# Performance work log

Measured on AMD Instinct MI355X. Metric: run time of the kernel, lower is better.

Reference implementation:

```python
import jax, jax.numpy as jnp
import numpy as np

KS = 3            # kernel_size
DILS = (1, 2, 4)  # dilation_list == padding_list
EPS = 1e-5        # BN eps


def _unfold3(x, d):
    # emulate F.unfold(kernel=3, dilation=d, padding=d, stride=1).view(b, c, 9, h, w)
    b, c, h, w = x.shape
    xp = jnp.pad(x, ((0, 0), (0, 0), (d, d), (d, d)))
    pats = [xp[:, :, i * d:i * d + h, j * d:j * d + w] for i in range(KS) for j in range(KS)]
    return jnp.stack(pats, axis=2)


def _conv1x1(x, w, b):
    return jnp.einsum('bchw,oc->bohw', x, w) + b[None, :, None, None]


def _bn_relu(x, g, be, m, v):
    s = g / jnp.sqrt(v + EPS)
    return jax.nn.relu(x * s[None, :, None, None] + (be - m * s)[None, :, None, None])


def _proj(x, w1, b1, g1, be1, m1, v1, w2, b2, g2, be2, m2, v2):
    h = _bn_relu(_conv1x1(x, w1, b1), g1, be1, m1, v1)
    return _bn_relu(_conv1x1(h, w2, b2), g2, be2, m2, v2)


def setup_inputs():
    key = jax.random.key(0)
    Cin, Ck, Cv, Cout = 512, 256, 256, 512
    B, H, W = 4, 64, 64
    ks = iter(jax.random.split(key, 48))

    def nrm(shape, s=0.02):
        return jax.random.normal(next(ks), shape, jnp.float32) * s

    def bn(c):
        return (jnp.ones((c,), jnp.float32) + nrm((c,), 0.1),  # gamma
                nrm((c,), 0.1),                                 # beta
                nrm((c,), 0.1),                                 # running mean
                jax.random.uniform(next(ks), (c,), jnp.float32, 0.5, 1.5))  # running var

    inp = {"x": jax.random.normal(next(ks), (B, Cin, H, W), jnp.float32)}
    for p in ("k", "q"):
        g1, be1, m1, v1 = bn(Ck)
        g2, be2, m2, v2 = bn(Ck)
        inp.update({
            p + "1_w": nrm((Ck, Cin)), p + "1_b": nrm((Ck,)),
            p + "1_g": g1, p + "1_be": be1, p + "1_m": m1, p + "1_v": v1,
            p + "2_w": nrm((Ck, Ck)), p + "2_b": nrm((Ck,)),
            p + "2_g": g2, p + "2_be": be2, p + "2_m": m2, p + "2_v": v2,
        })
    inp["v_w"] = nrm((Cv, Cin)); inp["v_b"] = nrm((Cv,))
    inp["w_w"] = nrm((Cout, Cv)); inp["w_b"] = nrm((Cout,))
    return inp


def reference(x,
              k1_w, k1_b, k1_g, k1_be, k1_m, k1_v,
              k2_w, k2_b, k2_g, k2_be, k2_m, k2_v,
              q1_w, q1_b, q1_g, q1_be, q1_m, q1_v,
              q2_w, q2_b, q2_g, q2_be, q2_m, q2_v,
              v_w, v_b, w_w, w_b):
    # scale == 1: MaxPool2d(1x1-equivalent) and final bilinear resize are identities.
    value = _conv1x1(x, v_w, v_b)                                  # (b,cv,h,w)
    keyf = _proj(x, k1_w, k1_b, k1_g, k1_be, k1_m, k1_v,
                 k2_w, k2_b, k2_g, k2_be, k2_m, k2_v)              # (b,ck,h,w)
    query = _proj(x, q1_w, q1_b, q1_g, q1_be, q1_m, q1_v,
                  q2_w, q2_b, q2_g, q2_be, q2_m, q2_v)             # (b,ck,h,w)
    uk = jnp.concatenate([_unfold3(keyf, d) for d in DILS], axis=2)   # (b,ck,27,h,w)
    uv = jnp.concatenate([_unfold3(value, d) for d in DILS], axis=2)  # (b,cv,27,h,w)
    sim = jnp.sum(uk * query[:, :, None], axis=1, keepdims=True)      # (b,1,27,h,w)
    sim = jax.nn.softmax(sim, axis=2)
    context = jnp.sum(sim * uv, axis=2)                               # (b,cv,h,w)
    return _conv1x1(context, w_w, w_b)
```

## Files before the change

### kernel.cpp

```cpp
#include <hip/hip_runtime.h>

#define HW   4096
#define Hh   64
#define Ww   64
#define NB   27
#define EPSBN 1e-5f

typedef _Float16 f16x8 __attribute__((ext_vector_type(8)));
typedef _Float16 f16x4 __attribute__((ext_vector_type(4)));
typedef _Float16 f16x2 __attribute__((ext_vector_type(2)));
typedef float    f32x4 __attribute__((ext_vector_type(4)));

__device__ __forceinline__ void gld_lds16(const void* g, void* l) {
    __builtin_amdgcn_global_load_lds(
        (const __attribute__((address_space(1))) unsigned int*)g,
        (__attribute__((address_space(3))) unsigned int*)l, 16, 0, 0);
}

struct GJob {
    const _Float16* in;
    const float*    xf;
    const float*    w;
    const float* b; const float* g; const float* be; const float* m; const float* v;
    _Float16* oh;
    float*    of;
};

__global__ __launch_bounds__(512, 1)
void gemm_f(GJob J0, GJob J1, GJob J2, int stage, int K, int JO, int mode)
{
    __shared__ _Float16 As[2][3][4096];
    __shared__ _Float16 Bs[3][16384];

    const int tid  = threadIdx.x;
    const int lane = tid & 63;
    const int w8   = tid >> 6;
    const int lr   = lane & 15;
    const int lg   = lane >> 4;
    const int wq   = w8 & 3;
    const int ph   = w8 >> 2;

    const int bid = blockIdx.x;
    const int xcd = bid & 7;
    const int jj  = bid >> 3;
    const int nb  = xcd * 8 + (jj >> 2);
    const int u   = jj & 3;

    const int nA = (stage == 1) ? 3 : 2;
    int js0, js1, js2, ob0, ob1, ob2;
    if (stage == 1)      { js0 = 0; js1 = 1; js2 = 2; ob0 = ob1 = ob2 = u * 64; }
    else if (stage == 2) { js0 = js1 = js2 = (u >> 1); ob0 = (u & 1) * 128; ob1 = ob0 + 64; ob2 = ob1; }
    else                 { js0 = js1 = js2 = 0; ob0 = u * 128; ob1 = ob0 + 64; ob2 = ob1; }

#define JSEL(js, f) ((js) == 0 ? J0.f : ((js) == 1 ? J1.f : J2.f))
    const float* w0 = JSEL(js0, w);
    const float* w1 = JSEL(js1, w);
    const float* w2 = JSEL(js2, w);
    const float* b0 = JSEL(js0, b); const float* g0 = JSEL(js0, g);
    const float* be0 = JSEL(js0, be); const float* m0 = JSEL(js0, m); const float* v0 = JSEL(js0, v);
    const float* b1 = JSEL(js1, b); const float* g1 = JSEL(js1, g);
    const float* be1 = JSEL(js1, be); const float* m1 = JSEL(js1, m); const float* v1 = JSEL(js1, v);
    const float* b2 = JSEL(js2, b); const float* g2 = JSEL(js2, g);
    const float* be2 = JSEL(js2, be); const float* m2 = JSEL(js2, m); const float* v2 = JSEL(js2, v);
    _Float16* oh0 = JSEL(js0, oh); float* of0 = JSEL(js0, of);
    _Float16* oh1 = JSEL(js1, oh); float* of1 = JSEL(js1, of);
    _Float16* oh2 = JSEL(js2, oh); float* of2 = JSEL(js2, of);
    const _Float16* bIn = JSEL(js0, in);
    const float*    bXf = JSEL(js0, xf);
#undef JSEL

    const int scol = (((lane & 7) ^ (lane >> 3)) << 3);
    const int rowA = w8 * 8 + (lane >> 3);
    const float* aS0 = w0 + (size_t)(ob0 + rowA) * K + scol;
    const float* aS1 = w1 + (size_t)(ob1 + rowA) * K + scol;
    const float* aS2 = w2 + (size_t)(ob2 + rowA) * K + scol;
    const int aoffW  = w8 * 1024 + lane * 16;

    const int rowB = w8 * 32 + (lane >> 3);
    const _Float16* bS = bIn ? (bIn + (size_t)(nb * 256 + rowB) * K + scol) : nullptr;

    const int px   = tid & 255;
    const int chh  = tid >> 8;
    const int pgS  = nb * 256 + px;
    const float* xbase = bXf ? (bXf + (size_t)(pgS >> 12) * 512 * HW + (pgS & 4095)) : nullptr;
    const int bxk  = (px & 7) << 4;
    const bool f32B = (bXf != nullptr);

    float ar0[8], ar1[8], ar2[8];
    float fr[32];

    auto ISSUE_A = [&](int rd) {
        const int kb = rd * 64;
        *(float4*)&ar0[0] = *(const float4*)(aS0 + kb);
        *(float4*)&ar0[4] = *(const float4*)(aS0 + kb + 4);
        *(float4*)&ar1[0] = *(const float4*)(aS1 + kb);
        *(float4*)&ar1[4] = *(const float4*)(aS1 + kb + 4);
        if (nA > 2) {
            *(float4*)&ar2[0] = *(const float4*)(aS2 + kb);
            *(float4*)&ar2[4] = *(const float4*)(aS2 + kb + 4);
        }
    };
    auto WRITE_A = [&](int buf) {
        f16x8 h0, h1, h2;
        #pragma unroll
        for (int i2 = 0; i2 < 8; ++i2) h0[i2] = (_Float16)ar0[i2];
        #pragma unroll
        for (int i2 = 0; i2 < 8; ++i2) h1[i2] = (_Float16)ar1[i2];
        *(f16x8*)((char*)&As[buf][0][0] + aoffW) = h0;
        *(f16x8*)((char*)&As[buf][1][0] + aoffW) = h1;
        if (nA > 2) {
            #pragma unroll
            for (int i2 = 0; i2 < 8; ++i2) h2[i2] = (_Float16)ar2[i2];
            *(f16x8*)((char*)&As[buf][2][0] + aoffW) = h2;
        }
    };
    auto ISSUE_BX = [&](int rd) {
        const int cb = rd * 64 + chh * 32;
        #pragma unroll
        for (int i2 = 0; i2 < 32; ++i2)
            fr[i2] = xbase[(size_t)(cb + i2) * HW];
    };
    auto WRITE_BX = [&](int buf) {
        #pragma unroll
        for (int g4 = 0; g4 < 4; ++g4) {
            f16x8 hv;
            #pragma unroll
            for (int i2 = 0; i2 < 8; ++i2) hv[i2] = (_Float16)fr[g4 * 8 + i2];
            *(f16x8*)((char*)&Bs[buf][0] + px * 128 + ((chh * 64 + g4 * 16) ^ bxk)) = hv;
        }
    };
    auto STAGE_B16 = [&](int buf, int rd) {
        const int kb = rd * 64;
        #pragma unroll
        for (int j2 = 0; j2 < 4; ++j2)
            gld_lds16(bS + (size_t)j2 * 8 * K + kb, (char*)&Bs[buf][0] + w8 * 4096 + j2 * 1024);
    };

    f32x4 acc0[8] = {}, acc1[8] = {}, acc2[8] = {};
    const int nr = K >> 6;

    auto MFMA_TILE = [&](int bb, int ab) {
        #pragma unroll
        for (int ks = 0; ks < 2; ++ks) {
            const int colx = (ks * 64 + lg * 16) ^ ((lr & 7) << 4);
            f16x8 bfr[8];
            #pragma unroll
            for (int t = 0; t < 8; ++t)
                bfr[t] = *(const f16x8*)((const char*)&Bs[bb][0] + (ph * 128 + t * 16 + lr) * 128 + colx);
            const int aoff = (wq * 16 + lr) * 128 + colx;
            const f16x8 af0 = *(const f16x8*)((const char*)&As[ab][0][0] + aoff);
            const f16x8 af1 = *(const f16x8*)((const char*)&As[ab][1][0] + aoff);
            #pragma unroll
            for (int t = 0; t < 8; ++t)
                acc0[t] = __builtin_amdgcn_mfma_f32_16x16x32_f16(af0, bfr[t], acc0[t], 0, 0, 0);
            #pragma unroll
            for (int t = 0; t < 8; ++t)
                acc1[t] = __builtin_amdgcn_mfma_f32_16x16x32_f16(af1, bfr[t], acc1[t], 0, 0, 0);
            if (nA > 2) {
                const f16x8 af2 = *(const f16x8*)((const char*)&As[ab][2][0] + aoff);
                #pragma unroll
                for (int t = 0; t < 8; ++t)
                    acc2[t] = __builtin_amdgcn_mfma_f32_16x16x32_f16(af2, bfr[t], acc2[t], 0, 0, 0);
            }
        }
    };

    if (f32B) {
        ISSUE_A(0);
        ISSUE_BX(0);
        WRITE_BX(0);
        WRITE_A(0);
        __syncthreads();
        int cur = 0;
        for (int rd = 0; rd < nr; ++rd) {
            const bool more = (rd + 1 < nr);
            if (more) {
                ISSUE_A(rd + 1);
                ISSUE_BX(rd + 1);
            }
            MFMA_TILE(cur, cur);
            if (more) {
                WRITE_A(cur ^ 1);
                WRITE_BX(cur ^ 1);
            }
            __syncthreads();
            cur ^= 1;
        }
    } else {
        STAGE_B16(0, 0);
        ISSUE_A(0);
        STAGE_B16(1, 1);
        WRITE_A(0);
        asm volatile("s_waitcnt vmcnt(4) lgkmcnt(0)" ::: "memory");
        __builtin_amdgcn_s_barrier();
        __builtin_amdgcn_sched_barrier(0);

        for (int rd = 0; rd < nr; ++rd) {
            const bool m1 = (rd + 1 < nr);
            const bool m2 = (rd + 2 < nr);
            if (m1) ISSUE_A(rd + 1);
            if (m2) STAGE_B16((rd + 2) % 3, rd + 2);
            MFMA_TILE(rd % 3, rd & 1);
            if (m1) WRITE_A((rd + 1) & 1);
            if (m2) asm volatile("s_waitcnt vmcnt(4) lgkmcnt(0)" ::: "memory");
            else    asm volatile("s_waitcnt vmcnt(0) lgkmcnt(0)" ::: "memory");
            __builtin_amdgcn_s_barrier();
            __builtin_amdgcn_sched_barrier(0);
        }
    }

#define EPI(accS, obS, bS_, gS, beS, mS, vS, ohS, ofS) do {                      \
        const int o4 = (obS) + wq * 16 + lg * 4;                                 \
        float sc[4], off[4];                                                     \
        _Pragma("unroll")                                                        \
        for (int r = 0; r < 4; ++r) {                                            \
            const int o = o4 + r;                                                \
            if (gS) { float s = (gS)[o] * rsqrtf((vS)[o] + EPSBN);               \
                      sc[r] = s; off[r] = fmaf((bS_)[o] - (mS)[o], s, (beS)[o]); }\
            else    { sc[r] = 1.f; off[r] = (bS_)[o]; }                          \
        }                                                                        \
        _Pragma("unroll")                                                        \
        for (int t = 0; t < 8; ++t) {                                            \
            const int pg = nb * 256 + ph * 128 + t * 16 + lr;                    \
            float vv[4];                                                         \
            _Pragma("unroll")                                                    \
            for (int r = 0; r < 4; ++r) {                                        \
                float tv = fmaf(accS[t][r], sc[r], off[r]);                      \
                vv[r] = (gS) ? fmaxf(tv, 0.f) : tv;                              \
            }                                                                    \
            if (mode == 0) {                                                     \
                f16x4 hh;                                                        \
                _Pragma("unroll")                                                \
                for (int r = 0; r < 4; ++r) hh[r] = (_Float16)vv[r];             \
                *(f16x4*)((ohS) + (size_t)pg * JO + o4) = hh;                    \
            } else {                                                             \
                _Pragma("unroll")                                                \
                for (int r = 0; r < 4; ++r)                                      \
                    (ofS)[((size_t)(pg >> 12) * JO + o4 + r) * HW + (pg & 4095)] = vv[r]; \
            }                                                                    \
        }                                                                        \
    } while (0)

    EPI(acc0, ob0, b0, g0, be0, m0, v0, oh0, of0);
    EPI(acc1, ob1, b1, g1, be1, m1, v1, oh1, of1);
    if (nA > 2) EPI(acc2, ob2, b2, g2, be2, m2, v2, oh2, of2);
#undef EPI
}

__global__ __launch_bounds__(256)
void attn_fused(const _Float16* __restrict__ keyT, const _Float16* __restrict__ qryT,
                const _Float16* __restrict__ valT, _Float16* __restrict__ ctxT)
{
    const int tid  = threadIdx.x;
    const int slot = tid & 31;
    const int b    = blockIdx.y;
    const int p    = blockIdx.x * 8 + (tid >> 5);
    const int y    = p >> 6;
    const int xc   = p & 63;

    int   idx[NB];
    float valf[NB];
    #pragma unroll
    for (int n = 0; n < NB; ++n) {
        const int d  = (n < 9) ? 1 : (n < 18 ? 2 : 4);
        const int i  = (n / 3) % 3 - 1;
        const int j  = n % 3 - 1;
        const int yy = y + i * d, xx = xc + j * d;
        const bool ok = ((unsigned)yy < (unsigned)Hh) && ((unsigned)xx < (unsigned)Ww);
        idx[n]  = min(max(yy, 0), Hh - 1) * Ww + min(max(xx, 0), Ww - 1);
        valf[n] = ok ? 1.f : 0.f;
    }

    const size_t base = (size_t)b * HW * 256 + slot * 8;
    const f16x8 q8 = *(const f16x8*)(qryT + base + (size_t)p * 256);

    f16x2 qp[4];
    qp[0] = __builtin_shufflevector(q8, q8, 0, 1);
    qp[1] = __builtin_shufflevector(q8, q8, 2, 3);
    qp[2] = __builtin_shufflevector(q8, q8, 4, 5);
    qp[3] = __builtin_shufflevector(q8, q8, 6, 7);

    float sim[NB];
    #pragma unroll
    for (int n = 0; n < NB; ++n) {
        const f16x8 k8 = *(const f16x8*)(keyT + base + (size_t)idx[n] * 256);
        float s = 0.f;
        s = __builtin_amdgcn_fdot2(__builtin_shufflevector(k8, k8, 0, 1), qp[0], s, false);
        s = __builtin_amdgcn_fdot2(__builtin_shufflevector(k8, k8, 2, 3), qp[1], s, false);
        s = __builtin_amdgcn_fdot2(__builtin_shufflevector(k8, k8, 4, 5), qp[2], s, false);
        s = __builtin_amdgcn_fdot2(__builtin_shufflevector(k8, k8, 6, 7), qp[3], s, false);
        sim[n] = s;
    }

    #pragma unroll
    for (int n = 0; n < NB; ++n) {
        float s = sim[n];
        s += __shfl_xor(s, 1);
        s += __shfl_xor(s, 2);
        s += __shfl_xor(s, 4);
        s += __shfl_xor(s, 8);
        s += __shfl_xor(s, 16);
        sim[n] = s * valf[n];
    }

    float mx = sim[0];
    #pragma unroll
    for (int n = 1; n < NB; ++n) mx = fmaxf(mx, sim[n]);
    float sum = 0.f;
    #pragma unroll
    for (int n = 0; n < NB; ++n) { sim[n] = __expf(sim[n] - mx); sum += sim[n]; }
    const float inv = 1.f / sum;
    #pragma unroll
    for (int n = 0; n < NB; ++n) sim[n] = sim[n] * inv * valf[n];

    float acc[8];
    #pragma unroll
    for (int i = 0; i < 8; ++i) acc[i] = 0.f;
    #pragma unroll
    for (int n = 0; n < NB; ++n) {
        const f16x8 v8 = *(const f16x8*)(valT + base + (size_t)idx[n] * 256);
        const float w = sim[n];
        #pragma unroll
        for (int i = 0; i < 8; ++i) acc[i] = fmaf(w, (float)v8[i], acc[i]);
    }

    f16x8 h;
    #pragma unroll
    for (int i = 0; i < 8; ++i) h[i] = (_Float16)acc[i];
    *(f16x8*)(ctxT + base + (size_t)p * 256) = h;
}

extern "C" void kernel_launch(void* const* d_in, const int* in_sizes, int n_in,
                              void* d_out, int out_size, void* d_ws, size_t ws_size,
                              hipStream_t stream)
{
    (void)in_sizes; (void)n_in; (void)out_size; (void)ws_size;
    const float* x     = (const float*)d_in[0];
    const float* k1_w  = (const float*)d_in[1];
    const float* k1_b  = (const float*)d_in[2];
    const float* k1_g  = (const float*)d_in[3];
    const float* k1_be = (const float*)d_in[4];
    const float* k1_m  = (const float*)d_in[5];
    const float* k1_v  = (const float*)d_in[6];
    const float* k2_w  = (const float*)d_in[7];
    const float* k2_b  = (const float*)d_in[8];
    const float* k2_g  = (const float*)d_in[9];
    const float* k2_be = (const float*)d_in[10];
    const float* k2_m  = (const float*)d_in[11];
    const float* k2_v  = (const float*)d_in[12];
    const float* q1_w  = (const float*)d_in[13];
    const float* q1_b  = (const float*)d_in[14];
    const float* q1_g  = (const float*)d_in[15];
    const float* q1_be = (const float*)d_in[16];
    const float* q1_m  = (const float*)d_in[17];
    const float* q1_v  = (const float*)d_in[18];
    const float* q2_w  = (const float*)d_in[19];
    const float* q2_b  = (const float*)d_in[20];
    const float* q2_g  = (const float*)d_in[21];
    const float* q2_be = (const float*)d_in[22];
    const float* q2_m  = (const float*)d_in[23];
    const float* q2_v  = (const float*)d_in[24];
    const float* v_w   = (const float*)d_in[25];
    const float* v_b   = (const float*)d_in[26];
    const float* w_w   = (const float*)d_in[27];
    const float* w_b   = (const float*)d_in[28];

    _Float16* hw = (_Float16*)d_ws;
    const size_t SH = (size_t)4 * HW * 256;
    _Float16* k1T   = hw;
    _Float16* q1T   = k1T + SH;
    _Float16* valT  = q1T + SH;
    _Float16* ctxT  = valT + SH;
    _Float16* keyPC = ctxT + SH;
    _Float16* qryPC = keyPC + SH;

    GJob jv  = { nullptr, x, v_w,  v_b,  nullptr, nullptr, nullptr, nullptr, valT,  nullptr };
    GJob jk1 = { nullptr, x, k1_w, k1_b, k1_g, k1_be, k1_m, k1_v,            k1T,   nullptr };
    GJob jq1 = { nullptr, x, q1_w, q1_b, q1_g, q1_be, q1_m, q1_v,            q1T,   nullptr };
    GJob jk2 = { k1T, nullptr, k2_w, k2_b, k2_g, k2_be, k2_m, k2_v,          keyPC, nullptr };
    GJob jq2 = { q1T, nullptr, q2_w, q2_b, q2_g, q2_be, q2_m, q2_v,          qryPC, nullptr };
    GJob jw  = { ctxT, nullptr, w_w, w_b,  nullptr, nullptr, nullptr, nullptr, nullptr, (float*)d_out };

    gemm_f<<<256, 512, 0, stream>>>(jv, jk1, jq1, 1, 512, 256, 0);
    gemm_f<<<256, 512, 0, stream>>>(jk2, jq2, jq2, 2, 256, 256, 0);
    attn_fused<<<dim3(512, 4), 256, 0, stream>>>(keyPC, qryPC, valT, ctxT);
    gemm_f<<<256, 512, 0, stream>>>(jw, jw, jw, 4, 256, 512, 2);
}
```

Before: 84.32 us.

## Pre-transpose x to fp16 pixel-major and use async LDS staging in first GEMM

```diff
diff --git a/kernel.cpp b/kernel.cpp
--- a/kernel.cpp
+++ b/kernel.cpp
@@ -17,9 +17,36 @@
         (__attribute__((address_space(3))) unsigned int*)l, 16, 0, 0);
 }
 
+__global__ __launch_bounds__(256)
+void prep_x(const float* __restrict__ x, _Float16* __restrict__ xT)
+{
+    __shared__ _Float16 T[64][516];
+    const int t  = blockIdx.x;
+    const int p0 = (t & 63) * 64;
+    const int b  = t >> 6;
+    const int tx = threadIdx.x & 63;
+    const int ty = threadIdx.x >> 6;
+
+    #pragma unroll 2
+    for (int ch = 0; ch < 16; ++ch) {
+        const int c0 = ch * 32 + ty * 8;
+        const float* xp = x + ((size_t)b * 512 + c0) * HW + p0 + tx;
+        f16x8 h;
+        #pragma unroll
+        for (int i = 0; i < 8; ++i) h[i] = (_Float16)xp[(size_t)i * HW];
+        *(f16x8*)&T[tx][c0] = h;
+    }
+    __syncthreads();
+    #pragma unroll 4
+    for (int rr = 0; rr < 16; ++rr) {
+        const int row = rr * 4 + ty;
+        f16x8 h = *(const f16x8*)&T[row][tx * 8];
+        *(f16x8*)(xT + ((size_t)b * HW + p0 + row) * 512 + tx * 8) = h;
+    }
+}
+
 struct GJob {
     const _Float16* in;
-    const float*    xf;
     const float*    w;
     const float* b; const float* g; const float* be; const float* m; const float* v;
     _Float16* oh;
@@ -66,7 +93,6 @@
     _Float16* oh1 = JSEL(js1, oh); float* of1 = JSEL(js1, of);
     _Float16* oh2 = JSEL(js2, oh); float* of2 = JSEL(js2, of);
     const _Float16* bIn = JSEL(js0, in);
-    const float*    bXf = JSEL(js0, xf);
 #undef JSEL
 
     const int scol = (((lane & 7) ^ (lane >> 3)) << 3);
@@ -77,17 +103,9 @@
     const int aoffW  = w8 * 1024 + lane * 16;
 
     const int rowB = w8 * 32 + (lane >> 3);
-    const _Float16* bS = bIn ? (bIn + (size_t)(nb * 256 + rowB) * K + scol) : nullptr;
-
-    const int px   = tid & 255;
-    const int chh  = tid >> 8;
-    const int pgS  = nb * 256 + px;
-    const float* xbase = bXf ? (bXf + (size_t)(pgS >> 12) * 512 * HW + (pgS & 4095)) : nullptr;
-    const int bxk  = (px & 7) << 4;
-    const bool f32B = (bXf != nullptr);
+    const _Float16* bS = bIn + (size_t)(nb * 256 + rowB) * K + scol;
 
     float ar0[8], ar1[8], ar2[8];
-    float fr[32];
 
     auto ISSUE_A = [&](int rd) {
         const int kb = rd * 64;
@@ -112,21 +130,6 @@
             #pragma unroll
             for (int i2 = 0; i2 < 8; ++i2) h2[i2] = (_Float16)ar2[i2];
             *(f16x8*)((char*)&As[buf][2][0] + aoffW) = h2;
-        }
-    };
-    auto ISSUE_BX = [&](int rd) {
-        const int cb = rd * 64 + chh * 32;
-        #pragma unroll
-        for (int i2 = 0; i2 < 32; ++i2)
-            fr[i2] = xbase[(size_t)(cb + i2) * HW];
-    };
-    auto WRITE_BX = [&](int buf) {
-        #pragma unroll
-        for (int g4 = 0; g4 < 4; ++g4) {
-            f16x8 hv;
-            #pragma unroll
-            for (int i2 = 0; i2 < 8; ++i2) hv[i2] = (_Float16)fr[g4 * 8 + i2];
-            *(f16x8*)((char*)&Bs[buf][0] + px * 128 + ((chh * 64 + g4 * 16) ^ bxk)) = hv;
         }
     };
     auto STAGE_B16 = [&](int buf, int rd) {
@@ -165,48 +168,25 @@
         }
     };
 
-    if (f32B) {
-        ISSUE_A(0);
-        ISSUE_BX(0);
-        WRITE_BX(0);
-        WRITE_A(0);
-        __syncthreads();
-        int cur = 0;
-        for (int rd = 0; rd < nr; ++rd) {
-            const bool more = (rd + 1 < nr);
-            if (more) {
-                ISSUE_A(rd + 1);
-                ISSUE_BX(rd + 1);
-            }
-            MFMA_TILE(cur, cur);
-            if (more) {
-                WRITE_A(cur ^ 1);
-                WRITE_BX(cur ^ 1);
-            }
-            __syncthreads();
-            cur ^= 1;
-        }
-    } else {
-        STAGE_B16(0, 0);
-        ISSUE_A(0);
-        STAGE_B16(1, 1);
-        WRITE_A(0);
-        asm volatile("s_waitcnt vmcnt(4) lgkmcnt(0)" ::: "memory");
+    STAGE_B16(0, 0);
+    ISSUE_A(0);
+    STAGE_B16(1, 1);
+    WRITE_A(0);
+    asm volatile("s_waitcnt vmcnt(4) lgkmcnt(0)" ::: "memory");
+    __builtin_amdgcn_s_barrier();
+    __builtin_amdgcn_sched_barrier(0);
+
+    for (int rd = 0; rd < nr; ++rd) {
+        const bool m1 = (rd + 1 < nr);
+        const bool m2 = (rd + 2 < nr);
+        if (m1) ISSUE_A(rd + 1);
+        if (m2) STAGE_B16((rd + 2) % 3, rd + 2);
+        MFMA_TILE(rd % 3, rd & 1);
+        if (m1) WRITE_A((rd + 1) & 1);
+        if (m2) asm volatile("s_waitcnt vmcnt(4) lgkmcnt(0)" ::: "memory");
+        else    asm volatile("s_waitcnt vmcnt(0) lgkmcnt(0)" ::: "memory");
         __builtin_amdgcn_s_barrier();
         __builtin_amdgcn_sched_barrier(0);
-
-        for (int rd = 0; rd < nr; ++rd) {
-            const bool m1 = (rd + 1 < nr);
-            const bool m2 = (rd + 2 < nr);
-            if (m1) ISSUE_A(rd + 1);
-            if (m2) STAGE_B16((rd + 2) % 3, rd + 2);
-            MFMA_TILE(rd % 3, rd & 1);
-            if (m1) WRITE_A((rd + 1) & 1);
-            if (m2) asm volatile("s_waitcnt vmcnt(4) lgkmcnt(0)" ::: "memory");
-            else    asm volatile("s_waitcnt vmcnt(0) lgkmcnt(0)" ::: "memory");
-            __builtin_amdgcn_s_barrier();
-            __builtin_amdgcn_sched_barrier(0);
-        }
     }
 
 #define EPI(accS, obS, bS_, gS, beS, mS, vS, ohS, ofS) do {                      \
@@ -366,21 +346,24 @@
     const float* w_b   = (const float*)d_in[28];
 
     _Float16* hw = (_Float16*)d_ws;
+    const size_t SX = (size_t)4 * HW * 512;
     const size_t SH = (size_t)4 * HW * 256;
-    _Float16* k1T   = hw;
+    _Float16* xT    = hw;
+    _Float16* k1T   = xT + SX;
     _Float16* q1T   = k1T + SH;
     _Float16* valT  = q1T + SH;
     _Float16* ctxT  = valT + SH;
     _Float16* keyPC = ctxT + SH;
     _Float16* qryPC = keyPC + SH;
 
-    GJob jv  = { nullptr, x, v_w,  v_b,  nullptr, nullptr, nullptr, nullptr, valT,  nullptr };
-    GJob jk1 = { nullptr, x, k1_w, k1_b, k1_g, k1_be, k1_m, k1_v,            k1T,   nullptr };
-    GJob jq1 = { nullptr, x, q1_w, q1_b, q1_g, q1_be, q1_m, q1_v,            q1T,   nullptr };
-    GJob jk2 = { k1T, nullptr, k2_w, k2_b, k2_g, k2_be, k2_m, k2_v,          keyPC, nullptr };
-    GJob jq2 = { q1T, nullptr, q2_w, q2_b, q2_g, q2_be, q2_m, q2_v,          qryPC, nullptr };
-    GJob jw  = { ctxT, nullptr, w_w, w_b,  nullptr, nullptr, nullptr, nullptr, nullptr, (float*)d_out };
-
+    GJob jv  = { xT,  v_w,  v_b,  nullptr, nullptr, nullptr, nullptr, valT,  nullptr };
+    GJob jk1 = { xT,  k1_w, k1_b, k1_g, k1_be, k1_m, k1_v,            k1T,   nullptr };
+    GJob jq1 = { xT,  q1_w, q1_b, q1_g, q1_be, q1_m, q1_v,            q1T,   nullptr };
+    GJob jk2 = { k1T, k2_w, k2_b, k2_g, k2_be, k2_m, k2_v,            keyPC, nullptr };
+    GJob jq2 = { q1T, q2_w, q2_b, q2_g, q2_be, q2_m, q2_v,            qryPC, nullptr };
+    GJob jw  = { ctxT, w_w, w_b,  nullptr, nullptr, nullptr, nullptr, nullptr, (float*)d_out };
+
+    prep_x<<<256, 256, 0, stream>>>(x, xT);
     gemm_f<<<256, 512, 0, stream>>>(jv, jk1, jq1, 1, 512, 256, 0);
     gemm_f<<<256, 512, 0, stream>>>(jk2, jq2, jq2, 2, 256, 256, 0);
     attn_fused<<<dim3(512, 4), 256, 0, stream>>>(keyPC, qryPC, valT, ctxT);
```

Result: slower. 91.20 us (+8.2%).
